# Kernel tuning notes

Hardware: AMD Instinct MI355X
Metric: run time of the kernel (lower is better)

## Reference

```python
import jax, jax.numpy as jnp
import numpy as np
import math

B_GRAPHS = 256
L_NODES = 64
N_NODES = B_GRAPHS * L_NODES
N_EDGES = N_NODES * 4
HEADS = 8
D_INNER = 512
N_DAGS = 1
DIAMETER = 64


def setup_inputs() -> dict:
    key = jax.random.key(0)
    ks = jax.random.split(key, 8)
    x = jax.random.normal(ks[0], (N_NODES, D_INNER), jnp.float32)
    B = jax.random.normal(ks[1], (N_NODES, D_INNER), jnp.float32)
    C = jax.random.normal(ks[2], (N_NODES, D_INNER), jnp.float32)
    dt = jax.random.normal(ks[3], (N_NODES, N_DAGS * HEADS * 2), jnp.float32)
    dt_edge = jax.random.normal(ks[4], (N_EDGES, N_DAGS * HEADS), jnp.float32)
    # DAG edges: within each graph, src_local < dst_local (gap 1..7) -> strictly upper triangular
    u = jax.random.randint(ks[5], (N_EDGES,), 0, L_NODES - 1)
    gap = jax.random.randint(ks[6], (N_EDGES,), 1, 8)
    v = jnp.minimum(u + gap, L_NODES - 1)
    graph = jnp.arange(N_EDGES) // (N_EDGES // B_GRAPHS)
    edge_index = jnp.stack([graph * L_NODES + u, graph * L_NODES + v]).astype(jnp.int32)
    data_batch = (jnp.arange(N_NODES) // L_NODES).astype(jnp.int32)
    dag_masks = jnp.ones((N_DAGS, N_EDGES), jnp.float32)
    # dt_bias init as in module __init__ (inverse softplus of dt in [1e-3, 1e-1])
    rng = np.random.default_rng(0)
    dtv = np.exp(rng.uniform(size=(HEADS,)) * (math.log(0.1) - math.log(0.001)) + math.log(0.001))
    dtv = np.clip(dtv, 1e-4, None)
    dt_bias = jnp.asarray(dtv + np.log(-np.expm1(-dtv)), jnp.float32)
    D = jnp.ones((HEADS,), jnp.float32)
    return dict(x=x, B=B, C=C, dt=dt, dt_edge=dt_edge, dt_bias=dt_bias, D=D,
                dag_masks=dag_masks, edge_index=edge_index, data_batch=data_batch,
                diameter=DIAMETER)


def _repeated_squaring_inverse(A, diam):
    # (I - A)^{-1} = prod_k (I + A^{2^k}) for nilpotent A; O(log diam) matmuls
    j = 2 ** int(math.ceil(math.log2(diam)))
    I = jnp.eye(A.shape[-1], dtype=A.dtype)
    last = A
    M = I + A
    for _ in range(2, int(math.log2(j)) + 1):
        last = last @ last
        M = M @ (I + last)
    return M


def reference(x, B, C, dt, dt_edge, dt_bias, D, dag_masks, edge_index, data_batch, diameter):
    N, din = x.shape
    g, E = dag_masks.shape
    n = dt_bias.shape[0]
    b = int(data_batch[-1]) + 1
    l = N // b  # equal-size graphs -> dense batching is a reshape, mask all-True
    h = din // n
    src, dst = edge_index[0], edge_index[1]

    # dt_node: (N, g*n*c) -> (c, g, n, N); softplus(dt + bias)
    c = dt.shape[1] // (g * n)
    dtn = dt.reshape(N, g, n, c).transpose(3, 1, 2, 0)
    dtn = jax.nn.softplus(dtn + dt_bias[None, None, :, None])
    dte = dt_edge.reshape(E, g, n).transpose(1, 2, 0)  # (g,n,E)
    dte = jax.nn.softplus(dte + dt_bias[None, :, None])

    dt_s, dt_t = dtn[0], dtn[1]
    dt_sum = (dt_s[:, :, src] + dt_t[:, :, dst] + dte) / np.sqrt(3.0)  # (g,n,E)
    dt_exp = jnp.exp(-dt_sum)
    msk = dag_masks[:, None, :]
    dt_sum = dt_sum * msk
    dt_exp = dt_exp * msk

    # dense adjacency with per-edge attrs; note 'b l1 l2 (g n) -> b g n l2 l1' transpose
    b_e = src // l
    sl = src % l
    dl = dst % l
    attr = dt_exp.transpose(2, 0, 1).reshape(E, g * n)
    adj = jnp.zeros((b, l, l, g * n), x.dtype).at[b_e, sl, dl].add(attr)
    A = adj.reshape(b, l, l, g, n).transpose(0, 3, 4, 2, 1)  # (b,g,n,l,l)

    # normalize_mat: sqrt outer product of in-degree counts, clamped at 1
    ec = jnp.zeros((g, N), x.dtype).at[:, dst].add(dag_masks)
    ec_dense = ec.T.reshape(b, l, g)
    outer = jnp.sqrt(jnp.einsum('blg,btg->bglt', ec_dense, ec_dense))
    outer = jnp.where(outer < 1.0, 1.0, outer)
    A = A / outer[:, :, None]

    dnorm = jnp.zeros((g, n, N), x.dtype).at[:, :, dst].add(dt_sum)
    dnorm = dnorm.transpose(2, 0, 1).reshape(b, l, g, n).transpose(0, 2, 3, 1)  # (b,g,n,l)

    A2 = A.reshape(b, g * n, l, l).astype(jnp.float32)
    L = _repeated_squaring_inverse(A2, int(diameter))
    L = L.reshape(b, g, n, l, l) * dnorm[..., None]

    x4 = x.reshape(b, l, n, h).transpose(0, 2, 1, 3)  # (b,n,l,h)
    B3 = B.reshape(b, l, -1)
    C3 = C.reshape(b, l, -1)
    # y = einsum(C,L,B,x) with B/C broadcast over (g,n): fold C.B^T into L
    CB = jnp.einsum('bld,btd->blt', C3, B3)
    M = L * CB[:, None, None]
    y = jnp.einsum('bgnlt,bnth->bgnlh', M, x4)
    y = y + x4[:, None] * D[None, None, :, None, None]
    y = y.transpose(0, 3, 1, 2, 4).reshape(N, g, n * h)  # b g n l h -> (N, g, n*h)
    y = y.sum(axis=1) / np.sqrt(g)
    return y
```

## Files before the change

kernel.cpp:

```cpp
#include <hip/hip_runtime.h>
#include <math.h>

#define NGRAPH 256
#define HEADS  8
#define DIN    512
#define EPG    256
#define NEDGE  65536

typedef short bf16x8 __attribute__((ext_vector_type(8)));
typedef float f32x4 __attribute__((ext_vector_type(4)));

__device__ __forceinline__ float softplusf(float v) {
    return (v > 20.f) ? v : log1pf(expf(v));
}
__device__ __forceinline__ unsigned short f2bf(float f) {
    union { float f; unsigned u; } c; c.f = f;
    unsigned r = c.u + 0x7fffu + ((c.u >> 16) & 1u);
    return (unsigned short)(r >> 16);
}
__device__ __forceinline__ float bf2f(unsigned short h) {
    union { float f; unsigned u; } c; c.u = ((unsigned)h) << 16;
    return c.f;
}
__device__ __forceinline__ int swz_idx(int row, int t) {
    int g = ((t >> 3) ^ (row ^ (row >> 3))) & 7;
    return (row << 6) | (g << 3) | (t & 7);
}
__device__ __forceinline__ void loadsplit(const float* p, bf16x8& hi, bf16x8& lo) {
    float4 u = *(const float4*)p;
    float4 v = *(const float4*)(p + 4);
    float vv[8] = {u.x, u.y, u.z, u.w, v.x, v.y, v.z, v.w};
    #pragma unroll
    for (int j = 0; j < 8; ++j) {
        union { float f; unsigned q; } c; c.f = vv[j];
        unsigned hb = c.q & 0xffff0000u;
        hi[j] = (short)(unsigned short)(hb >> 16);
        union { float f; unsigned q; } d; d.q = hb;
        union { float f; unsigned q; } e2; e2.f = vv[j] - d.f;
        lo[j] = (short)(unsigned short)(e2.q >> 16);
    }
}

__global__ __launch_bounds__(512, 2) void dag_fused_kernel(
        const float* __restrict__ x,
        const float* __restrict__ Bm,
        const float* __restrict__ Cm,
        const float* __restrict__ dt,
        const float* __restrict__ dt_edge,
        const float* __restrict__ dt_bias,
        const float* __restrict__ Dp,
        const float* __restrict__ dag_masks,
        const int* __restrict__ edge_index,
        float* __restrict__ out) {
    __shared__ unsigned short CBsh[64 * 68];
    __shared__ __align__(16) unsigned short Xt[HEADS][4096];
    __shared__ __align__(16) unsigned short Wl[HEADS][4096];
    __shared__ float Ab[HEADS][448];
    __shared__ float dts[HEADS][64];
    __shared__ float dtt[HEADS][64];
    __shared__ float dnsh[HEADS][64];
    __shared__ float ecsh[64];

    const int b = blockIdx.x;
    const int tid = threadIdx.x;
    const int w = tid >> 6;
    const int lane = tid & 63;
    const int lm = lane & 15;
    const int quad = lane >> 4;
    const float bias = dt_bias[w];

    {
        float2 dv = *(const float2*)(dt + ((size_t)(b * 64 + lane)) * 16 + w * 2);
        dts[w][lane] = softplusf(dv.x + bias);
        dtt[w][lane] = softplusf(dv.y + bias);
        dnsh[w][lane] = 0.f;
        #pragma unroll
        for (int s = 0; s < 7; ++s) Ab[w][lane * 7 + s] = 0.f;
        if (w == 0) ecsh[lane] = 0.f;
    }
    __syncthreads();

    if (tid < EPG) {
        int e = b * EPG + tid;
        atomicAdd(&ecsh[edge_index[NEDGE + e] & 63], dag_masks[e]);
    }
    {
        const int mi = w >> 1;
        const int ni0 = (w & 1) * 2;
        const float* Cr = Cm + ((size_t)(b * 64 + mi * 16 + lm)) * DIN + quad * 8;
        const float* B0 = Bm + ((size_t)(b * 64 + ni0 * 16 + lm)) * DIN + quad * 8;
        const float* B1 = B0 + (size_t)16 * DIN;
        f32x4 acc0 = {0.f, 0.f, 0.f, 0.f};
        f32x4 acc1 = {0.f, 0.f, 0.f, 0.f};
        #pragma unroll 4
        for (int ks = 0; ks < 16; ++ks) {
            bf16x8 ah, al, b0h, b0l, b1h, b1l;
            loadsplit(Cr + ks * 32, ah, al);
            loadsplit(B0 + ks * 32, b0h, b0l);
            loadsplit(B1 + ks * 32, b1h, b1l);
            acc0 = __builtin_amdgcn_mfma_f32_16x16x32_bf16(ah, b0h, acc0, 0, 0, 0);
            acc0 = __builtin_amdgcn_mfma_f32_16x16x32_bf16(ah, b0l, acc0, 0, 0, 0);
            acc0 = __builtin_amdgcn_mfma_f32_16x16x32_bf16(al, b0h, acc0, 0, 0, 0);
            acc1 = __builtin_amdgcn_mfma_f32_16x16x32_bf16(ah, b1h, acc1, 0, 0, 0);
            acc1 = __builtin_amdgcn_mfma_f32_16x16x32_bf16(ah, b1l, acc1, 0, 0, 0);
            acc1 = __builtin_amdgcn_mfma_f32_16x16x32_bf16(al, b1h, acc1, 0, 0, 0);
        }
        #pragma unroll
        for (int r = 0; r < 4; ++r) {
            int row = mi * 16 + quad * 4 + r;
            CBsh[row * 68 + ni0 * 16 + lm] = f2bf(acc0[r]);
            CBsh[row * 68 + (ni0 + 1) * 16 + lm] = f2bf(acc1[r]);
        }
    }
    {
        const float* xg = x + (size_t)b * 64 * DIN + w * 64;
        #pragma unroll 4
        for (int r = 0; r < 16; ++r) {
            int t = r * 4 + quad;
            int e0 = lm * 4;
            float4 v = *(const float4*)(xg + (size_t)t * DIN + e0);
            Xt[w][swz_idx(e0 + 0, t)] = f2bf(v.x);
            Xt[w][swz_idx(e0 + 1, t)] = f2bf(v.y);
            Xt[w][swz_idx(e0 + 2, t)] = f2bf(v.z);
            Xt[w][swz_idx(e0 + 3, t)] = f2bf(v.w);
        }
    }
    __syncthreads();

    {
        #pragma unroll
        for (int eo = 0; eo < 4; ++eo) {
            int e = b * EPG + eo * 64 + lane;
            int sl = edge_index[e] & 63;
            int dl = edge_index[NEDGE + e] & 63;
            float mk = dag_masks[e];
            float de = softplusf(dt_edge[(size_t)e * HEADS + w] + bias);
            float dsum = (dts[w][sl] + dtt[w][dl] + de) * 0.57735026918962576451f;
            float dexp = expf(-dsum);
            atomicAdd(&Ab[w][dl * 7 + (dl - sl - 1)], dexp * mk);
            atomicAdd(&dnsh[w][dl], dsum * mk);
        }
    }
    __syncthreads();

    {
        float eci = ecsh[lane];
        #pragma unroll
        for (int s = 0; s < 7; ++s) {
            int src = lane - 1 - s;
            if (src >= 0) {
                float den = sqrtf(eci * ecsh[src]);
                if (den < 1.f) den = 1.f;
                Ab[w][lane * 7 + s] = Ab[w][lane * 7 + s] / den;
            }
        }
    }
    __syncthreads();

    {
        const int j = lane;
        const float Dh = Dp[w];
        float mwin[7] = {0.f, 0.f, 0.f, 0.f, 0.f, 0.f, 0.f};
        const float* abp = &Ab[w][0];
        for (int i = 0; i < 64; ++i) {
            float mi_ = (j == i) ? 1.f : 0.f;
            #pragma unroll
            for (int s = 0; s < 7; ++s) mi_ += abp[i * 7 + s] * mwin[s];
            float wv = mi_ * bf2f(CBsh[i * 68 + j]) * dnsh[w][i];
            if (j == i) wv += Dh;
            Wl[w][swz_idx(i, j)] = f2bf(wv);
            #pragma unroll
            for (int s = 6; s > 0; --s) mwin[s] = mwin[s - 1];
            mwin[0] = mi_;
        }
    }
    __syncthreads();

    {
        bf16x8 af[4][2];
        #pragma unroll
        for (int mi = 0; mi < 4; ++mi) {
            int row0 = mi * 16 + lm;
            af[mi][0] = *(const bf16x8*)(&Wl[w][swz_idx(row0, quad * 8)]);
            af[mi][1] = *(const bf16x8*)(&Wl[w][swz_idx(row0, 32 + quad * 8)]);
        }
        float* og = out + (size_t)b * 64 * DIN + w * 64;
        #pragma unroll
        for (int eb = 0; eb < 4; ++eb) {
            int er = eb * 16 + lm;
            bf16x8 b0 = *(const bf16x8*)(&Xt[w][swz_idx(er, quad * 8)]);
            bf16x8 b1 = *(const bf16x8*)(&Xt[w][swz_idx(er, 32 + quad * 8)]);
            #pragma unroll
            for (int mi = 0; mi < 4; ++mi) {
                f32x4 acc = {0.f, 0.f, 0.f, 0.f};
                acc = __builtin_amdgcn_mfma_f32_16x16x32_bf16(af[mi][0], b0, acc, 0, 0, 0);
                acc = __builtin_amdgcn_mfma_f32_16x16x32_bf16(af[mi][1], b1, acc, 0, 0, 0);
                #pragma unroll
                for (int r = 0; r < 4; ++r) {
                    int row = mi * 16 + quad * 4 + r;
                    og[(size_t)row * DIN + eb * 16 + lm] = acc[r];
                }
            }
        }
    }
}

extern "C" void kernel_launch(void* const* d_in, const int* in_sizes, int n_in,
                              void* d_out, int out_size, void* d_ws, size_t ws_size,
                              hipStream_t stream) {
    (void)in_sizes; (void)n_in; (void)out_size; (void)d_ws; (void)ws_size;
    dag_fused_kernel<<<dim3(NGRAPH), dim3(512), 0, stream>>>(
        (const float*)d_in[0],
        (const float*)d_in[1],
        (const float*)d_in[2],
        (const float*)d_in[3],
        (const float*)d_in[4],
        (const float*)d_in[5],
        (const float*)d_in[6],
        (const float*)d_in[7],
        (const int*)d_in[8],
        (float*)d_out);
}
```

Measured before the change: 169.9 us.

## Split fused kernel into CB precompute plus per-head blocks

Moves the C·Bᵀ product into its own kernel that writes bf16 results to workspace. A second kernel then runs one 256-thread block per (graph, head) pair, giving 2048 blocks instead of 256 to improve occupancy and spread work across CUs. The cost is an extra launch, a workspace round-trip for CB, and eight redundant reads of the edge data per graph. The original fused kernel is kept as a fallback when the workspace is too small.

```diff
diff --git a/kernel.cpp b/kernel.cpp
--- a/kernel.cpp
+++ b/kernel.cpp
@@ -38,6 +38,162 @@
         union { float f; unsigned q; } d; d.q = hb;
         union { float f; unsigned q; } e2; e2.f = vv[j] - d.f;
         lo[j] = (short)(unsigned short)(e2.q >> 16);
+    }
+}
+
+__global__ __launch_bounds__(256, 4) void cb_bf16_kernel(const float* __restrict__ Bm,
+                                                         const float* __restrict__ Cm,
+                                                         unsigned short* __restrict__ CBbf) {
+    const int b = blockIdx.x;
+    const int qi = blockIdx.y >> 1;
+    const int qj = blockIdx.y & 1;
+    const int tid = threadIdx.x;
+    const int w = tid >> 6;
+    const int lane = tid & 63;
+    const int lm = lane & 15;
+    const int quad = lane >> 4;
+    const int mi = qi * 2 + (w >> 1);
+    const int ni = qj * 2 + (w & 1);
+
+    const float* Cr = Cm + ((size_t)(b * 64 + mi * 16 + lm)) * DIN + quad * 8;
+    const float* Br = Bm + ((size_t)(b * 64 + ni * 16 + lm)) * DIN + quad * 8;
+    f32x4 acc = {0.f, 0.f, 0.f, 0.f};
+    #pragma unroll 4
+    for (int ks = 0; ks < 16; ++ks) {
+        bf16x8 ah, al, bh, bl;
+        loadsplit(Cr + ks * 32, ah, al);
+        loadsplit(Br + ks * 32, bh, bl);
+        acc = __builtin_amdgcn_mfma_f32_16x16x32_bf16(ah, bh, acc, 0, 0, 0);
+        acc = __builtin_amdgcn_mfma_f32_16x16x32_bf16(ah, bl, acc, 0, 0, 0);
+        acc = __builtin_amdgcn_mfma_f32_16x16x32_bf16(al, bh, acc, 0, 0, 0);
+    }
+    unsigned short* o = CBbf + (size_t)b * 4096;
+    #pragma unroll
+    for (int r = 0; r < 4; ++r)
+        o[(mi * 16 + quad * 4 + r) * 64 + ni * 16 + lm] = f2bf(acc[r]);
+}
+
+__global__ __launch_bounds__(256, 4) void dag_head_kernel(
+        const float* __restrict__ x,
+        const float* __restrict__ dt,
+        const float* __restrict__ dt_edge,
+        const float* __restrict__ dt_bias,
+        const float* __restrict__ Dp,
+        const float* __restrict__ dag_masks,
+        const int* __restrict__ edge_index,
+        const unsigned short* __restrict__ CBbf,
+        float* __restrict__ out) {
+    __shared__ __align__(16) unsigned short CBsh[4096];
+    __shared__ __align__(16) unsigned short Xt[4096];
+    __shared__ __align__(16) unsigned short Wl[4096];
+    __shared__ float Ab[448];
+    __shared__ float dts[64];
+    __shared__ float dtt[64];
+    __shared__ float dnsh[64];
+    __shared__ float ecsh[64];
+
+    const int b = blockIdx.x;
+    const int head = blockIdx.y;
+    const int tid = threadIdx.x;
+    const int w = tid >> 6;
+    const int lane = tid & 63;
+    const int lm = lane & 15;
+    const int quad = lane >> 4;
+    const float bias = dt_bias[head];
+
+    {
+        const float4* src = (const float4*)(CBbf + (size_t)b * 4096);
+        float4* dst = (float4*)CBsh;
+        dst[tid] = src[tid];
+        dst[256 + tid] = src[256 + tid];
+    }
+    if (tid < 64) {
+        float2 dv = *(const float2*)(dt + ((size_t)(b * 64 + tid)) * 16 + head * 2);
+        dts[tid] = softplusf(dv.x + bias);
+        dtt[tid] = softplusf(dv.y + bias);
+        dnsh[tid] = 0.f;
+        ecsh[tid] = 0.f;
+    }
+    for (int k = tid; k < 448; k += 256) Ab[k] = 0.f;
+    {
+        const float* xg = x + (size_t)b * 64 * DIN + head * 64;
+        #pragma unroll
+        for (int rr = 0; rr < 4; ++rr) {
+            int t = w * 16 + rr * 4 + quad;
+            int e0 = lm * 4;
+            float4 v = *(const float4*)(xg + (size_t)t * DIN + e0);
+            Xt[swz_idx(e0 + 0, t)] = f2bf(v.x);
+            Xt[swz_idx(e0 + 1, t)] = f2bf(v.y);
+            Xt[swz_idx(e0 + 2, t)] = f2bf(v.z);
+            Xt[swz_idx(e0 + 3, t)] = f2bf(v.w);
+        }
+    }
+    __syncthreads();
+
+    {
+        int e = b * EPG + tid;
+        int sl = edge_index[e] & 63;
+        int dl = edge_index[NEDGE + e] & 63;
+        float mk = dag_masks[e];
+        float de = softplusf(dt_edge[(size_t)e * HEADS + head] + bias);
+        float dsum = (dts[sl] + dtt[dl] + de) * 0.57735026918962576451f;
+        float dexp = expf(-dsum);
+        atomicAdd(&Ab[dl * 7 + (dl - sl - 1)], dexp * mk);
+        atomicAdd(&dnsh[dl], dsum * mk);
+        atomicAdd(&ecsh[dl], mk);
+    }
+    __syncthreads();
+
+    if (tid < 64) {
+        float eci = ecsh[tid];
+        #pragma unroll
+        for (int s = 0; s < 7; ++s) {
+            int src = tid - 1 - s;
+            if (src >= 0) {
+                float den = sqrtf(eci * ecsh[src]);
+                if (den < 1.f) den = 1.f;
+                Ab[tid * 7 + s] = Ab[tid * 7 + s] / den;
+            }
+        }
+    }
+    __syncthreads();
+
+    if (w == 0) {
+        const int j = lane;
+        const float Dh = Dp[head];
+        float mwin[7] = {0.f, 0.f, 0.f, 0.f, 0.f, 0.f, 0.f};
+        for (int i = 0; i < 64; ++i) {
+            float mi_ = (j == i) ? 1.f : 0.f;
+            #pragma unroll
+            for (int s = 0; s < 7; ++s) mi_ += Ab[i * 7 + s] * mwin[s];
+            float wv = mi_ * bf2f(CBsh[i * 64 + j]) * dnsh[i];
+            if (j == i) wv += Dh;
+            Wl[swz_idx(i, j)] = f2bf(wv);
+            #pragma unroll
+            for (int s = 6; s > 0; --s) mwin[s] = mwin[s - 1];
+            mwin[0] = mi_;
+        }
+    }
+    __syncthreads();
+
+    {
+        bf16x8 a0 = *(const bf16x8*)(&Wl[swz_idx(16 * w + lm, quad * 8)]);
+        bf16x8 a1 = *(const bf16x8*)(&Wl[swz_idx(16 * w + lm, 32 + quad * 8)]);
+        float* og = out + (size_t)b * 64 * DIN + head * 64;
+        #pragma unroll
+        for (int eb = 0; eb < 4; ++eb) {
+            int er = eb * 16 + lm;
+            bf16x8 b0 = *(const bf16x8*)(&Xt[swz_idx(er, quad * 8)]);
+            bf16x8 b1 = *(const bf16x8*)(&Xt[swz_idx(er, 32 + quad * 8)]);
+            f32x4 acc = {0.f, 0.f, 0.f, 0.f};
+            acc = __builtin_amdgcn_mfma_f32_16x16x32_bf16(a0, b0, acc, 0, 0, 0);
+            acc = __builtin_amdgcn_mfma_f32_16x16x32_bf16(a1, b1, acc, 0, 0, 0);
+            #pragma unroll
+            for (int r = 0; r < 4; ++r) {
+                int row = 16 * w + quad * 4 + r;
+                og[(size_t)row * DIN + eb * 16 + lm] = acc[r];
+            }
+        }
     }
 }
 
@@ -208,16 +364,27 @@
 extern "C" void kernel_launch(void* const* d_in, const int* in_sizes, int n_in,
                               void* d_out, int out_size, void* d_ws, size_t ws_size,
                               hipStream_t stream) {
-    (void)in_sizes; (void)n_in; (void)out_size; (void)d_ws; (void)ws_size;
-    dag_fused_kernel<<<dim3(NGRAPH), dim3(512), 0, stream>>>(
-        (const float*)d_in[0],
-        (const float*)d_in[1],
-        (const float*)d_in[2],
-        (const float*)d_in[3],
-        (const float*)d_in[4],
-        (const float*)d_in[5],
-        (const float*)d_in[6],
-        (const float*)d_in[7],
-        (const int*)d_in[8],
-        (float*)d_out);
-}
+    (void)in_sizes; (void)n_in; (void)out_size;
+    const float* x        = (const float*)d_in[0];
+    const float* Bm       = (const float*)d_in[1];
+    const float* Cm       = (const float*)d_in[2];
+    const float* dt       = (const float*)d_in[3];
+    const float* dt_edge  = (const float*)d_in[4];
+    const float* dt_bias  = (const float*)d_in[5];
+    const float* Dp       = (const float*)d_in[6];
+    const float* dag_mask = (const float*)d_in[7];
+    const int*   edge_idx = (const int*)d_in[8];
+    float* out = (float*)d_out;
+
+    const size_t CB_BYTES = (size_t)NGRAPH * 4096 * sizeof(unsigned short);
+
+    if (ws_size >= CB_BYTES) {
+        unsigned short* CBbf = (unsigned short*)d_ws;
+        cb_bf16_kernel<<<dim3(NGRAPH, 4), 256, 0, stream>>>(Bm, Cm, CBbf);
+        dag_head_kernel<<<dim3(NGRAPH, HEADS), 256, 0, stream>>>(
+            x, dt, dt_edge, dt_bias, Dp, dag_mask, edge_idx, CBbf, out);
+    } else {
+        dag_fused_kernel<<<dim3(NGRAPH), dim3(512), 0, stream>>>(
+            x, Bm, Cm, dt, dt_edge, dt_bias, Dp, dag_mask, edge_idx, out);
+    }
+}
```

Result: slower. 193.2 us (+13.7%).

## Drop block barriers around per-wave stages and pipeline the recurrence loop

Applied to the files above, without the earlier changes.

Removes four of the block-wide barriers and relies on each wavefront only touching its own per-head shared arrays. The in-degree count moves into the edge loop, done by wave 0. The serial 64-step recurrence that builds W now prefetches the next row's coefficients, CB value and dnorm into registers, and sums the seven terms as a shallower FMA tree. Smaller changes: exp and log go through exp2/log2 intrinsics, the normalisation uses rsqrt with a clamp instead of sqrt plus divide, and x is transposed into shared memory with packed 64-bit stores. The aim is less barrier stalling and LDS latency on a latency-bound kernel. The cost is a dependence on same-wave LDS ordering and slightly different floating-point rounding.

```diff
diff --git a/kernel.cpp b/kernel.cpp
--- a/kernel.cpp
+++ b/kernel.cpp
@@ -6,12 +6,16 @@
 #define DIN    512
 #define EPG    256
 #define NEDGE  65536
+#define LOG2E 1.44269504088896341f
+#define LN2   0.69314718055994531f
 
 typedef short bf16x8 __attribute__((ext_vector_type(8)));
 typedef float f32x4 __attribute__((ext_vector_type(4)));
 
 __device__ __forceinline__ float softplusf(float v) {
-    return (v > 20.f) ? v : log1pf(expf(v));
+    if (v > 20.f) return v;
+    float t = exp2f(v * LOG2E);
+    return LN2 * log2f(1.f + t);
 }
 __device__ __forceinline__ unsigned short f2bf(float f) {
     union { float f; unsigned u; } c; c.f = f;
@@ -41,7 +45,7 @@
     }
 }
 
-__global__ __launch_bounds__(512, 2) void dag_fused_kernel(
+__global__ __launch_bounds__(512, 2) void dag_fused_v2(
         const float* __restrict__ x,
         const float* __restrict__ Bm,
         const float* __restrict__ Cm,
@@ -78,12 +82,7 @@
         for (int s = 0; s < 7; ++s) Ab[w][lane * 7 + s] = 0.f;
         if (w == 0) ecsh[lane] = 0.f;
     }
-    __syncthreads();
-
-    if (tid < EPG) {
-        int e = b * EPG + tid;
-        atomicAdd(&ecsh[edge_index[NEDGE + e] & 63], dag_masks[e]);
-    }
+
     {
         const int mi = w >> 1;
         const int ni0 = (w & 1) * 2;
@@ -112,20 +111,32 @@
             CBsh[row * 68 + (ni0 + 1) * 16 + lm] = f2bf(acc1[r]);
         }
     }
+
     {
         const float* xg = x + (size_t)b * 64 * DIN + w * 64;
-        #pragma unroll 4
-        for (int r = 0; r < 16; ++r) {
-            int t = r * 4 + quad;
+        #pragma unroll
+        for (int r = 0; r < 4; ++r) {
+            int t0 = quad * 4 + r * 16;
             int e0 = lm * 4;
-            float4 v = *(const float4*)(xg + (size_t)t * DIN + e0);
-            Xt[w][swz_idx(e0 + 0, t)] = f2bf(v.x);
-            Xt[w][swz_idx(e0 + 1, t)] = f2bf(v.y);
-            Xt[w][swz_idx(e0 + 2, t)] = f2bf(v.z);
-            Xt[w][swz_idx(e0 + 3, t)] = f2bf(v.w);
-        }
-    }
-    __syncthreads();
+            float4 v0 = *(const float4*)(xg + (size_t)(t0 + 0) * DIN + e0);
+            float4 v1 = *(const float4*)(xg + (size_t)(t0 + 1) * DIN + e0);
+            float4 v2 = *(const float4*)(xg + (size_t)(t0 + 2) * DIN + e0);
+            float4 v3 = *(const float4*)(xg + (size_t)(t0 + 3) * DIN + e0);
+            float a0[4] = {v0.x, v0.y, v0.z, v0.w};
+            float a1[4] = {v1.x, v1.y, v1.z, v1.w};
+            float a2[4] = {v2.x, v2.y, v2.z, v2.w};
+            float a3[4] = {v3.x, v3.y, v3.z, v3.w};
+            #pragma unroll
+            for (int k = 0; k < 4; ++k) {
+                unsigned long long pk =
+                      (unsigned long long)f2bf(a0[k])
+                    | ((unsigned long long)f2bf(a1[k]) << 16)
+                    | ((unsigned long long)f2bf(a2[k]) << 32)
+                    | ((unsigned long long)f2bf(a3[k]) << 48);
+                *(unsigned long long*)(&Xt[w][swz_idx(e0 + k, t0)]) = pk;
+            }
+        }
+    }
 
     {
         #pragma unroll
@@ -136,11 +147,13 @@
             float mk = dag_masks[e];
             float de = softplusf(dt_edge[(size_t)e * HEADS + w] + bias);
             float dsum = (dts[w][sl] + dtt[w][dl] + de) * 0.57735026918962576451f;
-            float dexp = expf(-dsum);
+            float dexp = exp2f(-dsum * LOG2E);
             atomicAdd(&Ab[w][dl * 7 + (dl - sl - 1)], dexp * mk);
             atomicAdd(&dnsh[w][dl], dsum * mk);
-        }
-    }
+            if (w == 0) atomicAdd(&ecsh[dl], mk);
+        }
+    }
+
     __syncthreads();
 
     {
@@ -149,32 +162,50 @@
         for (int s = 0; s < 7; ++s) {
             int src = lane - 1 - s;
             if (src >= 0) {
-                float den = sqrtf(eci * ecsh[src]);
-                if (den < 1.f) den = 1.f;
-                Ab[w][lane * 7 + s] = Ab[w][lane * 7 + s] / den;
-            }
-        }
-    }
-    __syncthreads();
+                float p = eci * ecsh[src];
+                float f = fminf(1.f, rsqrtf(p));
+                Ab[w][lane * 7 + s] *= f;
+            }
+        }
+    }
 
     {
         const int j = lane;
         const float Dh = Dp[w];
         float mwin[7] = {0.f, 0.f, 0.f, 0.f, 0.f, 0.f, 0.f};
-        const float* abp = &Ab[w][0];
+        float cab[7];
+        #pragma unroll
+        for (int s = 0; s < 7; ++s) cab[s] = Ab[w][s];
+        float cbv = bf2f(CBsh[j]);
+        float dnv = dnsh[w][0];
         for (int i = 0; i < 64; ++i) {
-            float mi_ = (j == i) ? 1.f : 0.f;
-            #pragma unroll
-            for (int s = 0; s < 7; ++s) mi_ += abp[i * 7 + s] * mwin[s];
-            float wv = mi_ * bf2f(CBsh[i * 68 + j]) * dnsh[w][i];
+            float nab[7], ncb = 0.f, ndn = 0.f;
+            if (i < 63) {
+                #pragma unroll
+                for (int s = 0; s < 7; ++s) nab[s] = Ab[w][(i + 1) * 7 + s];
+                ncb = bf2f(CBsh[(i + 1) * 68 + j]);
+                ndn = dnsh[w][i + 1];
+            } else {
+                #pragma unroll
+                for (int s = 0; s < 7; ++s) nab[s] = 0.f;
+            }
+            float diag = (j == i) ? 1.f : 0.f;
+            float t0 = fmaf(cab[0], mwin[0], fmaf(cab[1], mwin[1], diag));
+            float t1 = fmaf(cab[2], mwin[2], fmaf(cab[3], mwin[3], cab[4] * mwin[4]));
+            float t2 = fmaf(cab[5], mwin[5], cab[6] * mwin[6]);
+            float mi_ = t0 + (t1 + t2);
+            float wv = mi_ * cbv * dnv;
             if (j == i) wv += Dh;
             Wl[w][swz_idx(i, j)] = f2bf(wv);
             #pragma unroll
             for (int s = 6; s > 0; --s) mwin[s] = mwin[s - 1];
             mwin[0] = mi_;
-        }
-    }
-    __syncthreads();
+            #pragma unroll
+            for (int s = 0; s < 7; ++s) cab[s] = nab[s];
+            cbv = ncb;
+            dnv = ndn;
+        }
+    }
 
     {
         bf16x8 af[4][2];
@@ -209,7 +240,7 @@
                               void* d_out, int out_size, void* d_ws, size_t ws_size,
                               hipStream_t stream) {
     (void)in_sizes; (void)n_in; (void)out_size; (void)d_ws; (void)ws_size;
-    dag_fused_kernel<<<dim3(NGRAPH), dim3(512), 0, stream>>>(
+    dag_fused_v2<<<dim3(NGRAPH), dim3(512), 0, stream>>>(
         (const float*)d_in[0],
         (const float*)d_in[1],
         (const float*)d_in[2],
```

Result: faster. 165.8 us (-2.4%).
